# Optimization experiments

Measured on AMD Instinct MI355X. Metric: run time of the kernel, lower is better.

## Reference

```python
import jax, jax.numpy as jnp
import numpy as np

D_MODEL = 1024
N_HEADS = 16
DEPTH = D_MODEL // N_HEADS
B, S = 2, 2048
EPS_LN = 1e-6
EPS_KL = 2e-8


def _dense(x, W, b):
    return x @ W + b


def _ln(x, g, b):
    mu = jnp.mean(x, axis=-1, keepdims=True)
    var = jnp.mean(jnp.square(x - mu), axis=-1, keepdims=True)
    return (x - mu) * jax.lax.rsqrt(var + EPS_LN) * g + b


def _split_heads(x):
    # (B,S,D_MODEL) -> (B,H,S,DEPTH)
    return x.reshape(B, S, N_HEADS, DEPTH).transpose(0, 2, 1, 3)


def setup_inputs() -> dict:
    key = jax.random.key(0)
    ks = jax.random.split(key, 12)
    sc = 1.0 / np.sqrt(D_MODEL)
    inp = {
        'q_in': jax.random.normal(ks[0], (B, S, D_MODEL), jnp.float32),
        'k_in': jax.random.normal(ks[1], (B, S, D_MODEL), jnp.float32),
        'Wq': jax.random.normal(ks[2], (D_MODEL, D_MODEL), jnp.float32) * sc,
        'bq': jnp.zeros((D_MODEL,), jnp.float32),
        'Wk': jax.random.normal(ks[3], (D_MODEL, D_MODEL), jnp.float32) * sc,
        'bk': jnp.zeros((D_MODEL,), jnp.float32),
        'Wv': jax.random.normal(ks[4], (D_MODEL, D_MODEL), jnp.float32) * sc,
        'bv': jnp.zeros((D_MODEL,), jnp.float32),
        'Wo': jax.random.normal(ks[5], (D_MODEL, D_MODEL), jnp.float32) * sc,
        'bo': jnp.zeros((D_MODEL,), jnp.float32),
        'g1': jnp.ones((D_MODEL,), jnp.float32), 'b1': jnp.zeros((D_MODEL,), jnp.float32),
        'g2': jnp.ones((D_MODEL,), jnp.float32), 'b2': jnp.zeros((D_MODEL,), jnp.float32),
        'g3': jnp.ones((D_MODEL,), jnp.float32), 'b3': jnp.zeros((D_MODEL,), jnp.float32),
    }
    return inp


def reference(q_in, k_in, Wq, bq, Wk, bk, Wv, bv, Wo, bo, g1, b1, g2, b2, g3, b3):
    # Faithful to source: Wq applied twice to q, Wk twice to k, v = Wv(Wk(k_in))
    q = _ln(_dense(_dense(q_in, Wq, bq), Wq, bq), g1, b1)
    k1 = _dense(k_in, Wk, bk)
    k = _ln(_dense(k1, Wk, bk), g2, b2)
    v = _ln(_dense(k1, Wv, bv), g3, b3)

    q = _split_heads(q)   # (B,H,S,DEPTH)
    k = _split_heads(k)
    v = _split_heads(v)

    # KL-divergence attention scores.
    q_prob = jax.nn.softmax(q, axis=-1)
    k_prob = jax.nn.softmax(k, axis=-1)
    # sum_d q_prob*(log q_prob - log(k_prob+eps))
    # = [sum_d q_prob*log q_prob] - q_prob @ log(k_prob+eps)^T  (no 5D tensor)
    ent = jnp.sum(q_prob * jnp.log(q_prob), axis=-1)                     # (B,H,Sq)
    cross = jnp.einsum('bhqd,bhkd->bhqk', q_prob, jnp.log(k_prob + EPS_KL))
    kl_scores = ent[..., None] - cross                                   # (B,H,Sq,Sk)
    logits = kl_scores / jnp.sqrt(jnp.float32(DEPTH))

    # Csch softmax: csch(x)/sum csch(x)
    csch = 1.0 / jnp.sinh(logits)
    attn = csch / jnp.sum(csch, axis=-1, keepdims=True)                  # (B,H,Sq,Sk)

    out = jnp.einsum('bhqk,bhkd->bhqd', attn, v)
    out = out.transpose(0, 2, 1, 3).reshape(B, S, D_MODEL)
    output = _dense(out, Wo, bo)
    return output, attn
```

## Files before the change

kernel.cpp:

```cpp
#include <hip/hip_runtime.h>
#include <cstddef>
#include <cstdint>

#define BS      2
#define SEQ     2048
#define DM      1024
#define NH      16
#define DEPTH   64
#define ROWS    (BS*SEQ)
#define BHS     (BS*NH*SEQ)

typedef unsigned short u16;
typedef __attribute__((ext_vector_type(8))) short short8v;
typedef __attribute__((ext_vector_type(4))) float f32x4;

#define SWZ(row, cb) ((((row) << 7)) | ((cb) ^ (((row) & 7) << 4)))

__device__ __forceinline__ u16 f2bf(float x) {
    unsigned u = __builtin_bit_cast(unsigned, x);
    unsigned r = u + 0x7FFFu + ((u >> 16) & 1u);
    return (u16)(r >> 16);
}
__device__ __forceinline__ float bf2f(u16 h) {
    unsigned u = ((unsigned)h) << 16;
    return __builtin_bit_cast(float, u);
}

__device__ __forceinline__ float fast_csch(float x) {
    float t    = __expf(x);
    float den  = fmaf(t, t, -1.0f);
    bool  sm   = fabsf(x) < 0.04f;
    float d    = sm ? x : den;
    float r    = __builtin_amdgcn_rcpf(d);
    float big  = 2.0f * t * r;
    float smal = fmaf(x, -(1.0f/6.0f), r);
    return sm ? smal : big;
}

__global__ __launch_bounds__(256) void wsplit4_kernel(
    const float* __restrict__ W0, const float* __restrict__ W1,
    const float* __restrict__ W2_, const float* __restrict__ W3,
    u16* __restrict__ H0, u16* __restrict__ L0, u16* __restrict__ H1, u16* __restrict__ L1,
    u16* __restrict__ H2, u16* __restrict__ L2, u16* __restrict__ H3, u16* __restrict__ L3)
{
    const float* W; u16* H; u16* L;
    switch (blockIdx.z) {
        case 0: W = W0; H = H0; L = L0; break;
        case 1: W = W1; H = H1; L = L1; break;
        case 2: W = W2_; H = H2; L = L2; break;
        default: W = W3; H = H3; L = L3; break;
    }
    __shared__ float tile[32][33];
    const int bn = blockIdx.x, bk = blockIdx.y;
    const int c = threadIdx.x & 31, r0 = threadIdx.x >> 5;
#pragma unroll
    for (int r = 0; r < 32; r += 8)
        tile[r0 + r][c] = W[(size_t)(bk*32 + r0 + r) * DM + bn*32 + c];
    __syncthreads();
#pragma unroll
    for (int r = 0; r < 32; r += 8) {
        float v = tile[c][r0 + r];
        u16 h = f2bf(v);
        size_t o = (size_t)(bn*32 + r0 + r) * DM + bk*32 + c;
        H[o] = h;
        L[o] = f2bf(v - bf2f(h));
    }
}

__global__ __launch_bounds__(256) void split_kernel(
    const float* __restrict__ X, u16* __restrict__ H, u16* __restrict__ L)
{
    int i = blockIdx.x * 256 + threadIdx.x;
    float4 v = ((const float4*)X)[i];
    u16 h0 = f2bf(v.x), h1 = f2bf(v.y), h2 = f2bf(v.z), h3 = f2bf(v.w);
    u16 l0 = f2bf(v.x - bf2f(h0)), l1 = f2bf(v.y - bf2f(h1));
    u16 l2 = f2bf(v.z - bf2f(h2)), l3 = f2bf(v.w - bf2f(h3));
    uint2 hh, ll;
    hh.x = (unsigned)h0 | ((unsigned)h1 << 16); hh.y = (unsigned)h2 | ((unsigned)h3 << 16);
    ll.x = (unsigned)l0 | ((unsigned)l1 << 16); ll.y = (unsigned)l2 | ((unsigned)l3 << 16);
    ((uint2*)H)[i] = hh;
    ((uint2*)L)[i] = ll;
}

__global__ __launch_bounds__(256) void bias2_kernel(
    const float* __restrict__ bq, const float* __restrict__ Wq,
    float* __restrict__ bq2)
{
    __shared__ float part[4][64];
    const int t = threadIdx.x;
    const int nl = t & 63, kk = t >> 6;
    const int n = blockIdx.x * 64 + nl;
    float acc = 0.0f;
#pragma unroll 8
    for (int k = kk*256; k < kk*256 + 256; ++k)
        acc = fmaf(bq[k], Wq[(size_t)k * DM + n], acc);
    part[kk][nl] = acc;
    __syncthreads();
    if (t < 64)
        bq2[blockIdx.x*64 + t] = part[0][t] + part[1][t] + part[2][t] + part[3][t]
                               + bq[blockIdx.x*64 + t];
}

template<int OUT_MODE>
__global__ __launch_bounds__(256) void gemm_mfma(
    const u16* __restrict__ Ah, const u16* __restrict__ Al,
    const u16* __restrict__ Bh, const u16* __restrict__ Bl,
    const float* __restrict__ bias, float* __restrict__ C,
    u16* __restrict__ Ch, u16* __restrict__ Cl)
{
    constexpr int K = 1024, N = 1024;
    __shared__ u16 AsH[128*40], AsL[128*40], BsH[64*40], BsL[64*40];

    const int t = threadIdx.x;
    const int m0 = blockIdx.y * 128;
    const int n0 = blockIdx.x * 64;
    const int lane = t & 63, w = t >> 6;
    const int wr = w >> 1, wc = w & 1;
    const int lr = lane & 15, lk = lane >> 4;

    f32x4 acc[4][2];
#pragma unroll
    for (int i = 0; i < 4; ++i)
#pragma unroll
        for (int j = 0; j < 2; ++j) acc[i][j] = (f32x4){0.f,0.f,0.f,0.f};

    for (int k0 = 0; k0 < K; k0 += 32) {
        __syncthreads();
#pragma unroll
        for (int r = 0; r < 2; ++r) {
            int s = r*256 + t;
            int row = s >> 2, c = s & 3;
            size_t g = (size_t)(m0 + row) * K + k0 + c*8;
            *(short8v*)&AsH[row*40 + c*8] = *(const short8v*)&Ah[g];
            *(short8v*)&AsL[row*40 + c*8] = *(const short8v*)&Al[g];
        }
        {
            int row = t >> 2, c = t & 3;
            size_t g = (size_t)(n0 + row) * K + k0 + c*8;
            *(short8v*)&BsH[row*40 + c*8] = *(const short8v*)&Bh[g];
            *(short8v*)&BsL[row*40 + c*8] = *(const short8v*)&Bl[g];
        }
        __syncthreads();

        short8v ah[4], al[4], bh[2], bl[2];
#pragma unroll
        for (int i = 0; i < 4; ++i) {
            int off = (wr*64 + i*16 + lr)*40 + lk*8;
            ah[i] = *(const short8v*)&AsH[off];
            al[i] = *(const short8v*)&AsL[off];
        }
#pragma unroll
        for (int j = 0; j < 2; ++j) {
            int off = (wc*32 + j*16 + lr)*40 + lk*8;
            bh[j] = *(const short8v*)&BsH[off];
            bl[j] = *(const short8v*)&BsL[off];
        }
        __builtin_amdgcn_s_setprio(1);
#pragma unroll
        for (int i = 0; i < 4; ++i)
#pragma unroll
            for (int j = 0; j < 2; ++j) {
                acc[i][j] = __builtin_amdgcn_mfma_f32_16x16x32_bf16(ah[i], bh[j], acc[i][j], 0, 0, 0);
                acc[i][j] = __builtin_amdgcn_mfma_f32_16x16x32_bf16(ah[i], bl[j], acc[i][j], 0, 0, 0);
                acc[i][j] = __builtin_amdgcn_mfma_f32_16x16x32_bf16(al[i], bh[j], acc[i][j], 0, 0, 0);
            }
        __builtin_amdgcn_s_setprio(0);
    }

    float bj[2];
#pragma unroll
    for (int j = 0; j < 2; ++j) bj[j] = bias ? bias[n0 + wc*32 + j*16 + lr] : 0.0f;
#pragma unroll
    for (int i = 0; i < 4; ++i)
#pragma unroll
        for (int j = 0; j < 2; ++j) {
            int col = n0 + wc*32 + j*16 + lr;
#pragma unroll
            for (int r = 0; r < 4; ++r) {
                int row = m0 + wr*64 + i*16 + lk*4 + r;
                float v = acc[i][j][r] + bj[j];
                size_t o = (size_t)row * N + col;
                if constexpr (OUT_MODE == 0) {
                    C[o] = v;
                } else {
                    u16 h = f2bf(v);
                    Ch[o] = h;
                    Cl[o] = f2bf(v - bf2f(h));
                }
            }
        }
}

template<int OUT_MODE>
__global__ __launch_bounds__(256) void gemm_f32a(
    const float* __restrict__ A,
    const u16* __restrict__ Bh, const u16* __restrict__ Bl,
    const float* __restrict__ bias, float* __restrict__ C,
    u16* __restrict__ Ch, u16* __restrict__ Cl)
{
    constexpr int K = 1024, N = 1024;
    __shared__ u16 AsH[128*40], AsL[128*40], BsH[64*40], BsL[64*40];

    const int t = threadIdx.x;
    const int m0 = blockIdx.y * 128;
    const int n0 = blockIdx.x * 64;
    const int lane = t & 63, w = t >> 6;
    const int wr = w >> 1, wc = w & 1;
    const int lr = lane & 15, lk = lane >> 4;

    f32x4 acc[4][2];
#pragma unroll
    for (int i = 0; i < 4; ++i)
#pragma unroll
        for (int j = 0; j < 2; ++j) acc[i][j] = (f32x4){0.f,0.f,0.f,0.f};

    for (int k0 = 0; k0 < K; k0 += 32) {
        __syncthreads();
#pragma unroll
        for (int r = 0; r < 2; ++r) {
            int j = r*256 + t;
            int row = j >> 2, c8 = j & 3;
            const float* src = &A[(size_t)(m0 + row) * K + k0 + c8*8];
            float4 a = *(const float4*)src;
            float4 b = *(const float4*)(src + 4);
            float xs[8] = {a.x,a.y,a.z,a.w,b.x,b.y,b.z,b.w};
            short8v hv, lv;
#pragma unroll
            for (int jj = 0; jj < 8; ++jj) {
                u16 h = f2bf(xs[jj]);
                hv[jj] = (short)h;
                lv[jj] = (short)f2bf(xs[jj] - bf2f(h));
            }
            *(short8v*)&AsH[row*40 + c8*8] = hv;
            *(short8v*)&AsL[row*40 + c8*8] = lv;
        }
        {
            int row = t >> 2, c = t & 3;
            size_t g = (size_t)(n0 + row) * K + k0 + c*8;
            *(short8v*)&BsH[row*40 + c*8] = *(const short8v*)&Bh[g];
            *(short8v*)&BsL[row*40 + c*8] = *(const short8v*)&Bl[g];
        }
        __syncthreads();

        short8v ah[4], al[4], bh[2], bl[2];
#pragma unroll
        for (int i = 0; i < 4; ++i) {
            int off = (wr*64 + i*16 + lr)*40 + lk*8;
            ah[i] = *(const short8v*)&AsH[off];
            al[i] = *(const short8v*)&AsL[off];
        }
#pragma unroll
        for (int j = 0; j < 2; ++j) {
            int off = (wc*32 + j*16 + lr)*40 + lk*8;
            bh[j] = *(const short8v*)&BsH[off];
            bl[j] = *(const short8v*)&BsL[off];
        }
        __builtin_amdgcn_s_setprio(1);
#pragma unroll
        for (int i = 0; i < 4; ++i)
#pragma unroll
            for (int j = 0; j < 2; ++j) {
                acc[i][j] = __builtin_amdgcn_mfma_f32_16x16x32_bf16(ah[i], bh[j], acc[i][j], 0, 0, 0);
                acc[i][j] = __builtin_amdgcn_mfma_f32_16x16x32_bf16(ah[i], bl[j], acc[i][j], 0, 0, 0);
                acc[i][j] = __builtin_amdgcn_mfma_f32_16x16x32_bf16(al[i], bh[j], acc[i][j], 0, 0, 0);
            }
        __builtin_amdgcn_s_setprio(0);
    }

    float bj[2];
#pragma unroll
    for (int j = 0; j < 2; ++j) bj[j] = bias ? bias[n0 + wc*32 + j*16 + lr] : 0.0f;
#pragma unroll
    for (int i = 0; i < 4; ++i)
#pragma unroll
        for (int j = 0; j < 2; ++j) {
            int col = n0 + wc*32 + j*16 + lr;
#pragma unroll
            for (int r = 0; r < 4; ++r) {
                int row = m0 + wr*64 + i*16 + lk*4 + r;
                float v = acc[i][j][r] + bj[j];
                size_t o = (size_t)row * N + col;
                if constexpr (OUT_MODE == 0) {
                    C[o] = v;
                } else {
                    u16 h = f2bf(v);
                    Ch[o] = h;
                    Cl[o] = f2bf(v - bf2f(h));
                }
            }
        }
}

template<int MODE>
__global__ __launch_bounds__(256) void ln_head_kernel(
    const float* __restrict__ X, const float* __restrict__ G,
    const float* __restrict__ Bt, u16* __restrict__ OA,
    u16* __restrict__ OB, float* __restrict__ ENT)
{
    const int row = blockIdx.x;
    const int tid = threadIdx.x;
    const float* x = X + (size_t)row * DM;
    float4 v = *(const float4*)&x[tid*4];

    float s  = v.x + v.y + v.z + v.w;
    float ss = v.x*v.x + v.y*v.y + v.z*v.z + v.w*v.w;
#pragma unroll
    for (int m = 1; m < 64; m <<= 1) { s += __shfl_xor(s, m); ss += __shfl_xor(ss, m); }
    __shared__ float redS[4], redQ[4];
    const int wave = tid >> 6, lane = tid & 63;
    if (lane == 0) { redS[wave] = s; redQ[wave] = ss; }
    __syncthreads();
    s  = redS[0] + redS[1] + redS[2] + redS[3];
    ss = redQ[0] + redQ[1] + redQ[2] + redQ[3];
    const float mu   = s * (1.0f / DM);
    const float var  = ss * (1.0f / DM) - mu * mu;
    const float rsig = rsqrtf(var + 1e-6f);

    float4 gv = *(const float4*)&G[tid*4];
    float4 bv = *(const float4*)&Bt[tid*4];
    float y0 = (v.x - mu) * rsig * gv.x + bv.x;
    float y1 = (v.y - mu) * rsig * gv.y + bv.y;
    float y2 = (v.z - mu) * rsig * gv.z + bv.z;
    float y3 = (v.w - mu) * rsig * gv.w + bv.w;

    const int b  = row >> 11;
    const int sl = row & (SEQ - 1);
    const int h  = tid >> 4;
    const size_t obase = (((size_t)(b*NH + h)) * SEQ + sl) * DEPTH + (tid & 15) * 4;

    if constexpr (MODE == 2) {
        unsigned w0 = (unsigned)f2bf(y0) | ((unsigned)f2bf(y1) << 16);
        unsigned w1 = (unsigned)f2bf(y2) | ((unsigned)f2bf(y3) << 16);
        *(uint2*)&OA[obase] = make_uint2(w0, w1);
    } else {
        float mx = fmaxf(fmaxf(y0, y1), fmaxf(y2, y3));
#pragma unroll
        for (int m = 1; m < 16; m <<= 1) mx = fmaxf(mx, __shfl_xor(mx, m, 16));
        float e0 = expf(y0 - mx), e1 = expf(y1 - mx), e2 = expf(y2 - mx), e3 = expf(y3 - mx);
        float se = e0 + e1 + e2 + e3;
#pragma unroll
        for (int m = 1; m < 16; m <<= 1) se += __shfl_xor(se, m, 16);
        float inv = 1.0f / se;
        float p0 = e0*inv, p1 = e1*inv, p2 = e2*inv, p3 = e3*inv;
        float o0, o1, o2, o3;
        if constexpr (MODE == 0) { o0 = p0; o1 = p1; o2 = p2; o3 = p3; }
        else {
            o0 = logf(p0 + 2e-8f); o1 = logf(p1 + 2e-8f);
            o2 = logf(p2 + 2e-8f); o3 = logf(p3 + 2e-8f);
        }
        u16 h0 = f2bf(o0), h1 = f2bf(o1), h2 = f2bf(o2), h3 = f2bf(o3);
        unsigned w0 = (unsigned)h0 | ((unsigned)h1 << 16);
        unsigned w1 = (unsigned)h2 | ((unsigned)h3 << 16);
        *(uint2*)&OA[obase] = make_uint2(w0, w1);
        u16 l0 = f2bf(o0 - bf2f(h0)), l1 = f2bf(o1 - bf2f(h1));
        u16 l2 = f2bf(o2 - bf2f(h2)), l3 = f2bf(o3 - bf2f(h3));
        w0 = (unsigned)l0 | ((unsigned)l1 << 16);
        w1 = (unsigned)l2 | ((unsigned)l3 << 16);
        *(uint2*)&OB[obase] = make_uint2(w0, w1);

        if constexpr (MODE == 0) {
            float lse = logf(se);
            float el = p0*(y0-mx-lse) + p1*(y1-mx-lse) + p2*(y2-mx-lse) + p3*(y3-mx-lse);
#pragma unroll
            for (int m = 1; m < 16; m <<= 1) el += __shfl_xor(el, m, 16);
            if ((tid & 15) == 0) ENT[((size_t)(b*NH + h)) * SEQ + sl] = el;
        }
    }
}

__global__ __launch_bounds__(256) void vtrans_kernel(
    const u16* __restrict__ Vb, u16* __restrict__ VT)
{
    __shared__ u16 T[256*72];
    const int bh = blockIdx.y;
    const int s0 = blockIdx.x * 256;
    const int t  = threadIdx.x;
#pragma unroll
    for (int i = 0; i < 8; ++i) {
        int c = i*256 + t;
        int s = c >> 3, d0 = (c & 7) * 8;
        *(short8v*)&T[s*72 + d0] =
            *(const short8v*)&Vb[((size_t)bh*SEQ + s0 + s)*DEPTH + d0];
    }
    __syncthreads();
#pragma unroll
    for (int i = 0; i < 8; ++i) {
        int c = i*256 + t;
        int d = c >> 5, sl0 = (c & 31) * 8;
        short8v v;
#pragma unroll
        for (int j = 0; j < 8; ++j) v[j] = (short)T[(sl0 + j)*72 + d];
        *(short8v*)&VT[((size_t)bh*DEPTH + d)*SEQ + s0 + sl0] = v;
    }
}

__global__ __launch_bounds__(256, 4) void attn6_kernel(
    const u16* __restrict__ QPh, const u16* __restrict__ QPl,
    const u16* __restrict__ LKh, const u16* __restrict__ LKl,
    const u16* __restrict__ VT, const float* __restrict__ ENT,
    float* __restrict__ ATTN, u16* __restrict__ OH, u16* __restrict__ OL)
{
    const int wg   = blockIdx.x;
    const int wgid = (wg & 7) * 128 + (wg >> 3);
    const int bh   = wgid >> 5;
    const int q0   = (wgid & 31) * 64;

    const int t  = threadIdx.x;
    const int l  = t & 63, w = t >> 6;
    const int lr = l & 15, lg = l >> 4;
    const size_t rbase = (size_t)bh * SEQ;

    __shared__ u16 KhS[64*64], KlS[64*64], VtS[64*64], PS[64*64];

    const int kr0 = t >> 3,           c0 = t & 7;
    const int kr1 = (256 + t) >> 3,   c1 = t & 7;
    const int wz0 = SWZ(kr0, c0*16), wz1 = SWZ(kr1, c1*16);

    short8v qh[2], ql[2];
#pragma unroll
    for (int d = 0; d < 2; ++d) {
        size_t g = (rbase + q0 + w*16 + lr) * DEPTH + d*32 + lg*8;
        qh[d] = *(const short8v*)&QPh[g];
        ql[d] = *(const short8v*)&QPl[g];
    }
    float e8[4];
#pragma unroll
    for (int r = 0; r < 4; ++r)
        e8[r] = ENT[rbase + q0 + w*16 + lg*4 + r] * 0.125f;

    {
        size_t g0 = (rbase + kr0) * DEPTH + c0*8;
        size_t g1 = (rbase + kr1) * DEPTH + c1*8;
        *(short8v*)((char*)KhS + wz0) = *(const short8v*)&LKh[g0];
        *(short8v*)((char*)KlS + wz0) = *(const short8v*)&LKl[g0];
        *(short8v*)((char*)KhS + wz1) = *(const short8v*)&LKh[g1];
        *(short8v*)((char*)KlS + wz1) = *(const short8v*)&LKl[g1];
    }
    __syncthreads();

    float rs[4] = {0.f, 0.f, 0.f, 0.f};
    for (int k0 = 0; k0 < SEQ; k0 += 64) {
        const bool more = (k0 + 64) < SEQ;
        short8v ph0, pl0, ph1, pl1;
        if (more) {
            size_t g0 = (rbase + k0 + 64 + kr0) * DEPTH + c0*8;
            size_t g1 = (rbase + k0 + 64 + kr1) * DEPTH + c1*8;
            ph0 = *(const short8v*)&LKh[g0]; pl0 = *(const short8v*)&LKl[g0];
            ph1 = *(const short8v*)&LKh[g1]; pl1 = *(const short8v*)&LKl[g1];
        }

        f32x4 acc[4];
#pragma unroll
        for (int f = 0; f < 4; ++f) acc[f] = (f32x4){0.f,0.f,0.f,0.f};
        __builtin_amdgcn_s_setprio(1);
#pragma unroll
        for (int f = 0; f < 4; ++f)
#pragma unroll
            for (int d = 0; d < 2; ++d) {
                int off = SWZ(f*16 + lr, d*64 + lg*16);
                short8v kbh = *(const short8v*)((const char*)KhS + off);
                short8v kbl = *(const short8v*)((const char*)KlS + off);
                acc[f] = __builtin_amdgcn_mfma_f32_16x16x32_bf16(qh[d], kbh, acc[f], 0, 0, 0);
                acc[f] = __builtin_amdgcn_mfma_f32_16x16x32_bf16(qh[d], kbl, acc[f], 0, 0, 0);
                acc[f] = __builtin_amdgcn_mfma_f32_16x16x32_bf16(ql[d], kbh, acc[f], 0, 0, 0);
            }
        __builtin_amdgcn_s_setprio(0);
#pragma unroll
        for (int f = 0; f < 4; ++f)
#pragma unroll
            for (int r = 0; r < 4; ++r)
                rs[r] += fast_csch(fmaf(acc[f][r], -0.125f, e8[r]));

        __syncthreads();
        if (more) {
            *(short8v*)((char*)KhS + wz0) = ph0;
            *(short8v*)((char*)KlS + wz0) = pl0;
            *(short8v*)((char*)KhS + wz1) = ph1;
            *(short8v*)((char*)KlS + wz1) = pl1;
            __syncthreads();
        }
    }
#pragma unroll
    for (int m = 1; m < 16; m <<= 1)
#pragma unroll
        for (int r = 0; r < 4; ++r) rs[r] += __shfl_xor(rs[r], m, 16);
    float inv[4];
#pragma unroll
    for (int r = 0; r < 4; ++r) inv[r] = 1.0f / rs[r];

    {
        size_t g0 = (rbase + kr0) * DEPTH + c0*8;
        size_t g1 = (rbase + kr1) * DEPTH + c1*8;
        *(short8v*)((char*)KhS + wz0) = *(const short8v*)&LKh[g0];
        *(short8v*)((char*)KlS + wz0) = *(const short8v*)&LKl[g0];
        *(short8v*)((char*)KhS + wz1) = *(const short8v*)&LKh[g1];
        *(short8v*)((char*)KlS + wz1) = *(const short8v*)&LKl[g1];
        size_t v0 = ((size_t)bh * DEPTH + kr0) * SEQ + c0*8;
        size_t v1 = ((size_t)bh * DEPTH + kr1) * SEQ + c1*8;
        *(short8v*)((char*)VtS + wz0) = *(const short8v*)&VT[v0];
        *(short8v*)((char*)VtS + wz1) = *(const short8v*)&VT[v1];
    }
    __syncthreads();

    f32x4 av[4];
#pragma unroll
    for (int nf = 0; nf < 4; ++nf) av[nf] = (f32x4){0.f,0.f,0.f,0.f};

    for (int k0 = 0; k0 < SEQ; k0 += 64) {
        const bool more = (k0 + 64) < SEQ;
        short8v ph0, pl0, ph1, pl1, pv0, pv1;
        if (more) {
            size_t g0 = (rbase + k0 + 64 + kr0) * DEPTH + c0*8;
            size_t g1 = (rbase + k0 + 64 + kr1) * DEPTH + c1*8;
            ph0 = *(const short8v*)&LKh[g0]; pl0 = *(const short8v*)&LKl[g0];
            ph1 = *(const short8v*)&LKh[g1]; pl1 = *(const short8v*)&LKl[g1];
            size_t v0 = ((size_t)bh * DEPTH + kr0) * SEQ + k0 + 64 + c0*8;
            size_t v1 = ((size_t)bh * DEPTH + kr1) * SEQ + k0 + 64 + c1*8;
            pv0 = *(const short8v*)&VT[v0];
            pv1 = *(const short8v*)&VT[v1];
        }

        f32x4 acc[4];
#pragma unroll
        for (int f = 0; f < 4; ++f) acc[f] = (f32x4){0.f,0.f,0.f,0.f};
        __builtin_amdgcn_s_setprio(1);
#pragma unroll
        for (int f = 0; f < 4; ++f)
#pragma unroll
            for (int d = 0; d < 2; ++d) {
                int off = SWZ(f*16 + lr, d*64 + lg*16);
                short8v kbh = *(const short8v*)((const char*)KhS + off);
                short8v kbl = *(const short8v*)((const char*)KlS + off);
                acc[f] = __builtin_amdgcn_mfma_f32_16x16x32_bf16(qh[d], kbh, acc[f], 0, 0, 0);
                acc[f] = __builtin_amdgcn_mfma_f32_16x16x32_bf16(qh[d], kbl, acc[f], 0, 0, 0);
                acc[f] = __builtin_amdgcn_mfma_f32_16x16x32_bf16(ql[d], kbh, acc[f], 0, 0, 0);
            }
        __builtin_amdgcn_s_setprio(0);

#pragma unroll
        for (int f = 0; f < 4; ++f)
#pragma unroll
            for (int r = 0; r < 4; ++r) {
                float c = fast_csch(fmaf(acc[f][r], -0.125f, e8[r]));
                float a = c * inv[r];
                int q = w*16 + lg*4 + r;
                ATTN[(rbase + q0 + q) * SEQ + k0 + f*16 + lr] = a;
                *(u16*)((char*)PS + SWZ(q, (f*16 + lr)*2)) = f2bf(a);
            }

        short8v pa[2];
#pragma unroll
        for (int ks = 0; ks < 2; ++ks)
            pa[ks] = *(const short8v*)((const char*)PS + SWZ(w*16 + lr, ks*64 + lg*16));
        __builtin_amdgcn_s_setprio(1);
#pragma unroll
        for (int nf = 0; nf < 4; ++nf)
#pragma unroll
            for (int ks = 0; ks < 2; ++ks) {
                short8v vb = *(const short8v*)((const char*)VtS + SWZ(nf*16 + lr, ks*64 + lg*16));
                av[nf] = __builtin_amdgcn_mfma_f32_16x16x32_bf16(pa[ks], vb, av[nf], 0, 0, 0);
            }
        __builtin_amdgcn_s_setprio(0);

        __syncthreads();
        if (more) {
            *(short8v*)((char*)KhS + wz0) = ph0;
            *(short8v*)((char*)KlS + wz0) = pl0;
            *(short8v*)((char*)KhS + wz1) = ph1;
            *(short8v*)((char*)KlS + wz1) = pl1;
            *(short8v*)((char*)VtS + wz0) = pv0;
            *(short8v*)((char*)VtS + wz1) = pv1;
            __syncthreads();
        }
    }

    const int b = bh >> 4, h = bh & (NH - 1);
#pragma unroll
    for (int nf = 0; nf < 4; ++nf)
#pragma unroll
        for (int r = 0; r < 4; ++r) {
            int q = w*16 + lg*4 + r;
            int d = nf*16 + lr;
            size_t o = ((size_t)(b * SEQ + q0 + q)) * DM + h * DEPTH + d;
            float v = av[nf][r];
            u16 hh = f2bf(v);
            OH[o] = hh;
            OL[o] = f2bf(v - bf2f(hh));
        }
}

extern "C" void kernel_launch(void* const* d_in, const int* in_sizes, int n_in,
                              void* d_out, int out_size, void* d_ws, size_t ws_size,
                              hipStream_t stream)
{
    const float* q_in = (const float*)d_in[0];
    const float* k_in = (const float*)d_in[1];
    const float* Wq = (const float*)d_in[2];
    const float* bq = (const float*)d_in[3];
    const float* Wk = (const float*)d_in[4];
    const float* bk = (const float*)d_in[5];
    const float* Wv = (const float*)d_in[6];
    const float* bvp = (const float*)d_in[7];
    const float* Wo = (const float*)d_in[8];
    const float* bo = (const float*)d_in[9];
    const float* g1 = (const float*)d_in[10];
    const float* b1 = (const float*)d_in[11];
    const float* g2 = (const float*)d_in[12];
    const float* b2 = (const float*)d_in[13];
    const float* g3 = (const float*)d_in[14];
    const float* b3 = (const float*)d_in[15];

    float* out0 = (float*)d_out;
    float* attn = out0 + (size_t)ROWS * DM;

    char* base = (char*)d_ws;
    const size_t SLOT = (size_t)ROWS * DM * 4;
    const size_t HALF = (size_t)ROWS * DM;
    float* S0f = (float*)(base);
    float* S1f = (float*)(base + SLOT);
    float* S2f = (float*)(base + 2*SLOT);
    float* S3f = (float*)(base + 3*SLOT);
    u16* S0h = (u16*)S0f; u16* S0l = S0h + HALF;
    u16* S1h = (u16*)S1f;
    u16* S3h = (u16*)S3f; u16* S3l = S3h + HALF;
    u16* QPh = (u16*)S3f; u16* QPl = QPh + HALF;
    u16* LKh = (u16*)S2f; u16* LKl = LKh + HALF;
    u16* Vb  = (u16*)S0f; u16* VTp = Vb + HALF;
    u16* OHp = (u16*)S1f; u16* OLp = OHp + HALF;
    u16* WqnH = S0h;
    u16* WqnL = S0h + (size_t)DM*DM;

    char* wbase = base + 4*SLOT;
    const size_t WSZ = (size_t)DM * DM * 2;
    u16* WqH = (u16*)(wbase);           u16* WqL = (u16*)(wbase + WSZ);
    u16* WkH = (u16*)(wbase + 2*WSZ);   u16* WkL = (u16*)(wbase + 3*WSZ);
    u16* WvH = (u16*)(wbase + 4*WSZ);   u16* WvL = (u16*)(wbase + 5*WSZ);
    u16* WoH = (u16*)(wbase + 6*WSZ);   u16* WoL = (u16*)(wbase + 7*WSZ);
    u16* W2H = (u16*)(wbase + 8*WSZ);   u16* W2L = (u16*)(wbase + 9*WSZ);
    float* ent = (float*)(wbase + 10*WSZ);
    float* bq2 = ent + BHS;

    const dim3 ggrid(DM/64, ROWS/128);
    const dim3 g2grid(DM/64, DM/128);

    wsplit4_kernel<<<dim3(32,32,4), 256, 0, stream>>>(
        Wq, Wk, Wv, Wo, WqH, WqL, WkH, WkL, WvH, WvL, WoH, WoL);
    split_kernel<<<DM*DM/(4*256), 256, 0, stream>>>(Wq, WqnH, WqnL);
    bias2_kernel<<<16, 256, 0, stream>>>(bq, Wq, bq2);
    gemm_mfma<1><<<g2grid, 256, 0, stream>>>(WqH, WqL, WqnH, WqnL, nullptr,
                                             nullptr, W2H, W2L);

    gemm_f32a<0><<<ggrid, 256, 0, stream>>>(q_in, W2H, W2L, bq2, S2f, nullptr, nullptr);
    gemm_f32a<1><<<ggrid, 256, 0, stream>>>(k_in, WkH, WkL, bk, nullptr, S3h, S3l);
    gemm_mfma<0><<<ggrid, 256, 0, stream>>>(S3h, S3l, WkH, WkL, bk, S0f, nullptr, nullptr);
    gemm_mfma<0><<<ggrid, 256, 0, stream>>>(S3h, S3l, WvH, WvL, bvp, S1f, nullptr, nullptr);

    ln_head_kernel<0><<<ROWS, 256, 0, stream>>>(S2f, g1, b1, QPh, QPl, ent);
    ln_head_kernel<1><<<ROWS, 256, 0, stream>>>(S0f, g2, b2, LKh, LKl, nullptr);
    ln_head_kernel<2><<<ROWS, 256, 0, stream>>>(S1f, g3, b3, Vb, nullptr, nullptr);
    vtrans_kernel<<<dim3(SEQ/256, BS*NH), 256, 0, stream>>>(Vb, VTp);

    attn6_kernel<<<dim3(SEQ/64 * BS*NH), 256, 0, stream>>>(
        QPh, QPl, LKh, LKl, VTp, ent, attn, OHp, OLp);

    gemm_mfma<0><<<ggrid, 256, 0, stream>>>(OHp, OLp, WoH, WoL, bo, out0, nullptr, nullptr);
}
```

Baseline: 605.1 us.

## Merge weight-prep kernels and drop register prefetch in attention loops

Combines the weight split, Wq plain split and bias-composition kernels into one launch by adding two extra grid z-slices. In the attention kernel, the register-staged prefetch of the next K/V tile is removed. Each iteration now loads its tile directly into shared memory between two barriers. This cuts register pressure and launch overhead, but global-load latency is no longer overlapped with the MFMA work of the previous tile. The merged launch also carries many idle blocks in the bias slice that return immediately.

```diff
diff --git a/kernel.cpp b/kernel.cpp
--- a/kernel.cpp
+++ b/kernel.cpp
@@ -37,14 +37,48 @@
     return sm ? smal : big;
 }
 
-__global__ __launch_bounds__(256) void wsplit4_kernel(
+__global__ __launch_bounds__(256) void wprep_kernel(
     const float* __restrict__ W0, const float* __restrict__ W1,
     const float* __restrict__ W2_, const float* __restrict__ W3,
+    const float* __restrict__ bq,
     u16* __restrict__ H0, u16* __restrict__ L0, u16* __restrict__ H1, u16* __restrict__ L1,
-    u16* __restrict__ H2, u16* __restrict__ L2, u16* __restrict__ H3, u16* __restrict__ L3)
+    u16* __restrict__ H2, u16* __restrict__ L2, u16* __restrict__ H3, u16* __restrict__ L3,
+    u16* __restrict__ HN, u16* __restrict__ LN_, float* __restrict__ bq2)
 {
+    const int z = blockIdx.z;
+    if (z == 4) {
+        int bid = blockIdx.y * 32 + blockIdx.x;
+        int i = bid * 256 + threadIdx.x;
+        float4 v = ((const float4*)W0)[i];
+        u16 h0 = f2bf(v.x), h1 = f2bf(v.y), h2 = f2bf(v.z), h3 = f2bf(v.w);
+        u16 l0 = f2bf(v.x - bf2f(h0)), l1 = f2bf(v.y - bf2f(h1));
+        u16 l2 = f2bf(v.z - bf2f(h2)), l3 = f2bf(v.w - bf2f(h3));
+        uint2 hh, ll;
+        hh.x = (unsigned)h0 | ((unsigned)h1 << 16); hh.y = (unsigned)h2 | ((unsigned)h3 << 16);
+        ll.x = (unsigned)l0 | ((unsigned)l1 << 16); ll.y = (unsigned)l2 | ((unsigned)l3 << 16);
+        ((uint2*)HN)[i] = hh;
+        ((uint2*)LN_)[i] = ll;
+        return;
+    }
+    if (z == 5) {
+        if (blockIdx.y != 0 || blockIdx.x >= 16) return;
+        __shared__ float part[4][64];
+        const int t = threadIdx.x;
+        const int nl = t & 63, kk = t >> 6;
+        const int n = blockIdx.x * 64 + nl;
+        float acc = 0.0f;
+#pragma unroll 8
+        for (int k = kk*256; k < kk*256 + 256; ++k)
+            acc = fmaf(bq[k], W0[(size_t)k * DM + n], acc);
+        part[kk][nl] = acc;
+        __syncthreads();
+        if (t < 64)
+            bq2[blockIdx.x*64 + t] = part[0][t] + part[1][t] + part[2][t] + part[3][t]
+                                   + bq[blockIdx.x*64 + t];
+        return;
+    }
     const float* W; u16* H; u16* L;
-    switch (blockIdx.z) {
+    switch (z) {
         case 0: W = W0; H = H0; L = L0; break;
         case 1: W = W1; H = H1; L = L1; break;
         case 2: W = W2_; H = H2; L = L2; break;
@@ -65,40 +99,6 @@
         H[o] = h;
         L[o] = f2bf(v - bf2f(h));
     }
-}
-
-__global__ __launch_bounds__(256) void split_kernel(
-    const float* __restrict__ X, u16* __restrict__ H, u16* __restrict__ L)
-{
-    int i = blockIdx.x * 256 + threadIdx.x;
-    float4 v = ((const float4*)X)[i];
-    u16 h0 = f2bf(v.x), h1 = f2bf(v.y), h2 = f2bf(v.z), h3 = f2bf(v.w);
-    u16 l0 = f2bf(v.x - bf2f(h0)), l1 = f2bf(v.y - bf2f(h1));
-    u16 l2 = f2bf(v.z - bf2f(h2)), l3 = f2bf(v.w - bf2f(h3));
-    uint2 hh, ll;
-    hh.x = (unsigned)h0 | ((unsigned)h1 << 16); hh.y = (unsigned)h2 | ((unsigned)h3 << 16);
-    ll.x = (unsigned)l0 | ((unsigned)l1 << 16); ll.y = (unsigned)l2 | ((unsigned)l3 << 16);
-    ((uint2*)H)[i] = hh;
-    ((uint2*)L)[i] = ll;
-}
-
-__global__ __launch_bounds__(256) void bias2_kernel(
-    const float* __restrict__ bq, const float* __restrict__ Wq,
-    float* __restrict__ bq2)
-{
-    __shared__ float part[4][64];
-    const int t = threadIdx.x;
-    const int nl = t & 63, kk = t >> 6;
-    const int n = blockIdx.x * 64 + nl;
-    float acc = 0.0f;
-#pragma unroll 8
-    for (int k = kk*256; k < kk*256 + 256; ++k)
-        acc = fmaf(bq[k], Wq[(size_t)k * DM + n], acc);
-    part[kk][nl] = acc;
-    __syncthreads();
-    if (t < 64)
-        bq2[blockIdx.x*64 + t] = part[0][t] + part[1][t] + part[2][t] + part[3][t]
-                               + bq[blockIdx.x*64 + t];
 }
 
 template<int OUT_MODE>
@@ -394,7 +394,7 @@
     }
 }
 
-__global__ __launch_bounds__(256, 4) void attn6_kernel(
+__global__ __launch_bounds__(256, 4) void attn5_kernel(
     const u16* __restrict__ QPh, const u16* __restrict__ QPl,
     const u16* __restrict__ LKh, const u16* __restrict__ LKl,
     const u16* __restrict__ VT, const float* __restrict__ ENT,
@@ -412,10 +412,6 @@
 
     __shared__ u16 KhS[64*64], KlS[64*64], VtS[64*64], PS[64*64];
 
-    const int kr0 = t >> 3,           c0 = t & 7;
-    const int kr1 = (256 + t) >> 3,   c1 = t & 7;
-    const int wz0 = SWZ(kr0, c0*16), wz1 = SWZ(kr1, c1*16);
-
     short8v qh[2], ql[2];
 #pragma unroll
     for (int d = 0; d < 2; ++d) {
@@ -428,26 +424,17 @@
     for (int r = 0; r < 4; ++r)
         e8[r] = ENT[rbase + q0 + w*16 + lg*4 + r] * 0.125f;
 
-    {
-        size_t g0 = (rbase + kr0) * DEPTH + c0*8;
-        size_t g1 = (rbase + kr1) * DEPTH + c1*8;
-        *(short8v*)((char*)KhS + wz0) = *(const short8v*)&LKh[g0];
-        *(short8v*)((char*)KlS + wz0) = *(const short8v*)&LKl[g0];
-        *(short8v*)((char*)KhS + wz1) = *(const short8v*)&LKh[g1];
-        *(short8v*)((char*)KlS + wz1) = *(const short8v*)&LKl[g1];
-    }
-    __syncthreads();
-
     float rs[4] = {0.f, 0.f, 0.f, 0.f};
     for (int k0 = 0; k0 < SEQ; k0 += 64) {
-        const bool more = (k0 + 64) < SEQ;
-        short8v ph0, pl0, ph1, pl1;
-        if (more) {
-            size_t g0 = (rbase + k0 + 64 + kr0) * DEPTH + c0*8;
-            size_t g1 = (rbase + k0 + 64 + kr1) * DEPTH + c1*8;
-            ph0 = *(const short8v*)&LKh[g0]; pl0 = *(const short8v*)&LKl[g0];
-            ph1 = *(const short8v*)&LKh[g1]; pl1 = *(const short8v*)&LKl[g1];
-        }
+        if (k0) __syncthreads();
+#pragma unroll
+        for (int r = 0; r < 2; ++r) {
+            int s = r*256 + t; int kr = s >> 3, cb = (s & 7) * 16;
+            size_t g = (rbase + k0 + kr) * DEPTH + (s & 7) * 8;
+            *(short8v*)((char*)KhS + SWZ(kr, cb)) = *(const short8v*)&LKh[g];
+            *(short8v*)((char*)KlS + SWZ(kr, cb)) = *(const short8v*)&LKl[g];
+        }
+        __syncthreads();
 
         f32x4 acc[4];
 #pragma unroll
@@ -470,15 +457,6 @@
 #pragma unroll
             for (int r = 0; r < 4; ++r)
                 rs[r] += fast_csch(fmaf(acc[f][r], -0.125f, e8[r]));
-
-        __syncthreads();
-        if (more) {
-            *(short8v*)((char*)KhS + wz0) = ph0;
-            *(short8v*)((char*)KlS + wz0) = pl0;
-            *(short8v*)((char*)KhS + wz1) = ph1;
-            *(short8v*)((char*)KlS + wz1) = pl1;
-            __syncthreads();
-        }
     }
 #pragma unroll
     for (int m = 1; m < 16; m <<= 1)
@@ -488,37 +466,26 @@
 #pragma unroll
     for (int r = 0; r < 4; ++r) inv[r] = 1.0f / rs[r];
 
-    {
-        size_t g0 = (rbase + kr0) * DEPTH + c0*8;
-        size_t g1 = (rbase + kr1) * DEPTH + c1*8;
-        *(short8v*)((char*)KhS + wz0) = *(const short8v*)&LKh[g0];
-        *(short8v*)((char*)KlS + wz0) = *(const short8v*)&LKl[g0];
-        *(short8v*)((char*)KhS + wz1) = *(const short8v*)&LKh[g1];
-        *(short8v*)((char*)KlS + wz1) = *(const short8v*)&LKl[g1];
-        size_t v0 = ((size_t)bh * DEPTH + kr0) * SEQ + c0*8;
-        size_t v1 = ((size_t)bh * DEPTH + kr1) * SEQ + c1*8;
-        *(short8v*)((char*)VtS + wz0) = *(const short8v*)&VT[v0];
-        *(short8v*)((char*)VtS + wz1) = *(const short8v*)&VT[v1];
-    }
-    __syncthreads();
-
     f32x4 av[4];
 #pragma unroll
     for (int nf = 0; nf < 4; ++nf) av[nf] = (f32x4){0.f,0.f,0.f,0.f};
 
     for (int k0 = 0; k0 < SEQ; k0 += 64) {
-        const bool more = (k0 + 64) < SEQ;
-        short8v ph0, pl0, ph1, pl1, pv0, pv1;
-        if (more) {
-            size_t g0 = (rbase + k0 + 64 + kr0) * DEPTH + c0*8;
-            size_t g1 = (rbase + k0 + 64 + kr1) * DEPTH + c1*8;
-            ph0 = *(const short8v*)&LKh[g0]; pl0 = *(const short8v*)&LKl[g0];
-            ph1 = *(const short8v*)&LKh[g1]; pl1 = *(const short8v*)&LKl[g1];
-            size_t v0 = ((size_t)bh * DEPTH + kr0) * SEQ + k0 + 64 + c0*8;
-            size_t v1 = ((size_t)bh * DEPTH + kr1) * SEQ + k0 + 64 + c1*8;
-            pv0 = *(const short8v*)&VT[v0];
-            pv1 = *(const short8v*)&VT[v1];
-        }
+        __syncthreads();
+#pragma unroll
+        for (int r = 0; r < 2; ++r) {
+            int s = r*256 + t; int kr = s >> 3, cb = (s & 7) * 16;
+            size_t g = (rbase + k0 + kr) * DEPTH + (s & 7) * 8;
+            *(short8v*)((char*)KhS + SWZ(kr, cb)) = *(const short8v*)&LKh[g];
+            *(short8v*)((char*)KlS + SWZ(kr, cb)) = *(const short8v*)&LKl[g];
+        }
+#pragma unroll
+        for (int r = 0; r < 2; ++r) {
+            int s = r*256 + t; int dd = s >> 3, cb = (s & 7) * 16;
+            *(short8v*)((char*)VtS + SWZ(dd, cb)) =
+                *(const short8v*)&VT[((size_t)bh * DEPTH + dd) * SEQ + k0 + (s & 7) * 8];
+        }
+        __syncthreads();
 
         f32x4 acc[4];
 #pragma unroll
@@ -561,17 +528,6 @@
                 av[nf] = __builtin_amdgcn_mfma_f32_16x16x32_bf16(pa[ks], vb, av[nf], 0, 0, 0);
             }
         __builtin_amdgcn_s_setprio(0);
-
-        __syncthreads();
-        if (more) {
-            *(short8v*)((char*)KhS + wz0) = ph0;
-            *(short8v*)((char*)KlS + wz0) = pl0;
-            *(short8v*)((char*)KhS + wz1) = ph1;
-            *(short8v*)((char*)KlS + wz1) = pl1;
-            *(short8v*)((char*)VtS + wz0) = pv0;
-            *(short8v*)((char*)VtS + wz1) = pv1;
-            __syncthreads();
-        }
     }
 
     const int b = bh >> 4, h = bh & (NH - 1);
@@ -620,8 +576,7 @@
     float* S1f = (float*)(base + SLOT);
     float* S2f = (float*)(base + 2*SLOT);
     float* S3f = (float*)(base + 3*SLOT);
-    u16* S0h = (u16*)S0f; u16* S0l = S0h + HALF;
-    u16* S1h = (u16*)S1f;
+    u16* S0h = (u16*)S0f;
     u16* S3h = (u16*)S3f; u16* S3l = S3h + HALF;
     u16* QPh = (u16*)S3f; u16* QPl = QPh + HALF;
     u16* LKh = (u16*)S2f; u16* LKl = LKh + HALF;
@@ -643,10 +598,9 @@
     const dim3 ggrid(DM/64, ROWS/128);
     const dim3 g2grid(DM/64, DM/128);
 
-    wsplit4_kernel<<<dim3(32,32,4), 256, 0, stream>>>(
-        Wq, Wk, Wv, Wo, WqH, WqL, WkH, WkL, WvH, WvL, WoH, WoL);
-    split_kernel<<<DM*DM/(4*256), 256, 0, stream>>>(Wq, WqnH, WqnL);
-    bias2_kernel<<<16, 256, 0, stream>>>(bq, Wq, bq2);
+    wprep_kernel<<<dim3(32,32,6), 256, 0, stream>>>(
+        Wq, Wk, Wv, Wo, bq,
+        WqH, WqL, WkH, WkL, WvH, WvL, WoH, WoL, WqnH, WqnL, bq2);
     gemm_mfma<1><<<g2grid, 256, 0, stream>>>(WqH, WqL, WqnH, WqnL, nullptr,
                                              nullptr, W2H, W2L);
 
@@ -660,7 +614,7 @@
     ln_head_kernel<2><<<ROWS, 256, 0, stream>>>(S1f, g3, b3, Vb, nullptr, nullptr);
     vtrans_kernel<<<dim3(SEQ/256, BS*NH), 256, 0, stream>>>(Vb, VTp);
 
-    attn6_kernel<<<dim3(SEQ/64 * BS*NH), 256, 0, stream>>>(
+    attn5_kernel<<<dim3(SEQ/64 * BS*NH), 256, 0, stream>>>(
         QPh, QPl, LKh, LKl, VTp, ent, attn, OHp, OLp);
 
     gemm_mfma<0><<<ggrid, 256, 0, stream>>>(OHp, OLp, WoH, WoL, bo, out0, nullptr, nullptr);
```

Result: faster. 573.6 us (-5.2%).
